# Kernel tuning notes

Hardware: AMD Instinct MI355X
Metric: run time of the kernel (lower is better)

## Reference

```python
import jax, jax.numpy as jnp
import numpy as np

FF = 2          # freqfold
HALF_FF = 1     # ff // 2

def _fold_k(t, G, ff):
    # t: [N, G, D] -> real/imag each [N, nband, G*ff]
    N, _, D = t.shape
    Df = D // 2
    nband = Df // ff
    t = jnp.swapaxes(t, -1, -2)  # [N, D, G]
    def fold(x):  # x: [N, Df, G]
        x = x.reshape(N, nband, ff, G).transpose(0, 2, 1, 3)  # [N, ff, nband, G]
        return x.reshape(N, nband, G * ff)
    return fold(t[:, :Df, :]), fold(t[:, Df:, :])

def _fold_q(t, G, groups, ff):
    # t: [N, H, D] with H = G*groups -> real/imag each [N, groups, nband, G*ff]
    N, H, D = t.shape
    Df = D // 2
    nband = Df // ff
    t = t.reshape(N, G, groups, D).transpose(0, 2, 1, 3)  # [N, groups, G, D]
    t = jnp.swapaxes(t, -1, -2)                            # [N, groups, D, G]
    def fold(x):  # x: [N, groups, Df, G]
        x = x.reshape(N, groups, nband, ff, G).transpose(0, 1, 3, 2, 4)  # [N, groups, ff, nband, G]
        return x.reshape(N, groups, nband, G * ff)
    return fold(t[:, :, :Df, :]), fold(t[:, :, Df:, :])

def setup_inputs() -> dict:
    key = jax.random.key(0)
    ks = jax.random.split(key, 8)
    N, H, G, D, r = 8192, 32, 8, 128, 4
    ff = FF
    nband = D // (2 * ff)
    gff = G * ff
    nope_in = G * D - D // 2
    return {
        "q": jax.random.normal(ks[0], (N, H, D), jnp.float32),
        "k": jax.random.normal(ks[1], (N, G, D), jnp.float32),
        "v": jax.random.normal(ks[2], (N, G, D), jnp.float32),
        "q_orig": jax.random.normal(ks[3], (N, H, D), jnp.float32),
        "k_orig": jax.random.normal(ks[4], (N, G, D), jnp.float32),
        "qk_index_proj": 0.02 * jax.random.normal(ks[5], (nband, gff, gff), jnp.float32),
        "qk_nope_proj_w": 0.02 * jax.random.normal(ks[6], (D // 2, nope_in), jnp.float32),
        "v_transform": 0.02 * jax.random.normal(ks[7], (H, D, r), jnp.float32),
    }

def reference(q, k, v, q_orig, k_orig, qk_index_proj, qk_nope_proj_w, v_transform):
    N, H, D = q.shape
    G = k.shape[1]
    groups = H // G
    ff, half_ff = FF, HALF_FF
    nband = D // (2 * ff)
    nope_cols = G * ff - half_ff
    qk_w = qk_index_proj

    # ---- rope path (post-RoPE q, k) ----
    kr_re, kr_im = _fold_k(k, G, ff)
    kr_re_p = jnp.einsum('bnf,nfr->bnr', kr_re, qk_w)
    kr_im_p = jnp.einsum('bnf,nfr->bnr', kr_im, qk_w)
    index_k_rope = jnp.concatenate([
        kr_re_p[:, :, :half_ff].reshape(N, nband * half_ff),
        kr_im_p[:, :, :half_ff].reshape(N, nband * half_ff)], axis=-1)

    qr_re, qr_im = _fold_q(q, G, groups, ff)
    qr_re_p = jnp.einsum('tgnf,nfr->tgnr', qr_re, qk_w)
    qr_im_p = jnp.einsum('tgnf,nfr->tgnr', qr_im, qk_w)
    index_q_rope = jnp.concatenate([
        qr_re_p[:, :, :, :half_ff].reshape(N, groups, nband * half_ff),
        qr_im_p[:, :, :, :half_ff].reshape(N, groups, nband * half_ff)], axis=-1)

    # ---- nope path (pre-RoPE q_orig, k_orig) ----
    kn_re, kn_im = _fold_k(k_orig, G, ff)
    kn_re_p = jnp.einsum('bnf,nfr->bnr', kn_re, qk_w)
    kn_im_p = jnp.einsum('bnf,nfr->bnr', kn_im, qk_w)
    k_nope_rotary = jnp.concatenate([
        kn_re_p[:, :, half_ff:].reshape(N, nband * nope_cols),
        kn_im_p[:, :, half_ff:].reshape(N, nband * nope_cols)], axis=-1)
    k_nope_lr = k_nope_rotary @ qk_nope_proj_w.T
    index_k = jnp.concatenate([index_k_rope, k_nope_lr], axis=-1)  # [N, D]

    qn_re, qn_im = _fold_q(q_orig, G, groups, ff)
    qn_re_p = jnp.einsum('tgnf,nfr->tgnr', qn_re, qk_w)
    qn_im_p = jnp.einsum('tgnf,nfr->tgnr', qn_im, qk_w)
    q_nope_rotary = jnp.concatenate([
        qn_re_p[:, :, :, half_ff:].reshape(N, groups, nband * nope_cols),
        qn_im_p[:, :, :, half_ff:].reshape(N, groups, nband * nope_cols)], axis=-1)
    q_nope_lr = q_nope_rotary @ qk_nope_proj_w.T
    index_q = jnp.concatenate([index_q_rope, q_nope_lr], axis=-1)  # [N, groups, D]

    # ---- per-head weights from V ----
    r = v_transform.shape[-1]
    v_h = jnp.repeat(v, groups, axis=1)  # [N, H, D]
    w = jnp.einsum('nhd,hdr->nhr', v_h, v_transform)
    w = w.reshape(N, G, groups, r).transpose(0, 2, 1, 3).reshape(N, groups, G * r)
    weights = jnp.linalg.norm(w.astype(jnp.float32), axis=-1)  # [N, groups]

    return index_q, index_k, weights
```

## Files before the change

### kernel.cpp

```cpp
#include <hip/hip_runtime.h>
#include <math.h>

namespace {
constexpr int N_TOK  = 8192;
constexpr int GROUPS = 4;
constexpr int D      = 128;
}

typedef short v8s __attribute__((ext_vector_type(8)));
typedef float v4f __attribute__((ext_vector_type(4)));

__device__ __forceinline__ short f2bf(float f) {
    union { float f; unsigned u; } x; x.f = f;
    unsigned r = x.u + 0x7FFFu + ((x.u >> 16) & 1u);
    return (short)(r >> 16);
}

__global__ __launch_bounds__(256)
void build_MT(const float* __restrict__ widx,
              const float* __restrict__ wn,
              short* __restrict__ MT)
{
    const int idx = blockIdx.x * 256 + threadIdx.x;
    const int col = idx >> 10;
    const int kk  = idx & 1023;
    const int g   = kk >> 7;
    const int dp  = kk & 127;
    const int part = dp >> 6;
    const int dpp  = dp & 63;
    const int B    = (dpp & 1) * 16 + (dpp >> 2);
    const int c    = g + 8 * ((dpp >> 1) & 1);

    float val;
    if (col < 64) {
        val = (col == part * 32 + B) ? widx[B * 256 + c * 16] : 0.f;
    } else {
        const int d2 = col - 64;
        const float* wrow = wn + d2 * 960 + part * 480 + B * 15;
        const float* wi   = widx + B * 256 + c * 16;
        float s = 0.f;
#pragma unroll
        for (int o = 1; o < 16; ++o) s += wi[o] * wrow[o - 1];
        val = s;
    }
    MT[idx] = f2bf(val);
}

__global__ __launch_bounds__(256)
void gemm_kernel(const float* __restrict__ q,
                 const float* __restrict__ k,
                 const float* __restrict__ q_orig,
                 const float* __restrict__ k_orig,
                 const short* __restrict__ MT,
                 float* __restrict__ out_iq,
                 float* __restrict__ out_ik)
{
    const int lane = threadIdx.x & 63;
    const int wave = threadIdx.x >> 6;
    const int m    = lane & 15;
    const int quad = lane >> 4;
    const int base_row = blockIdx.x * 64 + wave * 16;

    const int row = base_row + m;
    const int n   = row / 5;
    const int jj  = row - n * 5;
    const bool isq = (jj < 4);
    const float* ropep = isq ? (q      + n * 4096 + jj * 128) : (k      + n * 1024);
    const float* nopep = isq ? (q_orig + n * 4096 + jj * 128) : (k_orig + n * 1024);

    const short* bbase = MT + m * 1024;

    v4f acc[8];
#pragma unroll
    for (int t = 0; t < 8; ++t) acc[t] = (v4f){0.f, 0.f, 0.f, 0.f};

#pragma unroll 2
    for (int ks = 0; ks < 32; ++ks) {
        const int kk   = ks * 32 + quad * 8;
        const int offA = isq ? ((kk >> 7) * 512 + (kk & 127)) : kk;
        const float4 r0 = *(const float4*)(ropep + offA);
        const float4 r1 = *(const float4*)(ropep + offA + 4);
        const float4 n0 = *(const float4*)(nopep + offA);
        const float4 n1 = *(const float4*)(nopep + offA + 4);
        v8s ar, an;
        ar[0] = f2bf(r0.x); ar[1] = f2bf(r0.y); ar[2] = f2bf(r0.z); ar[3] = f2bf(r0.w);
        ar[4] = f2bf(r1.x); ar[5] = f2bf(r1.y); ar[6] = f2bf(r1.z); ar[7] = f2bf(r1.w);
        an[0] = f2bf(n0.x); an[1] = f2bf(n0.y); an[2] = f2bf(n0.z); an[3] = f2bf(n0.w);
        an[4] = f2bf(n1.x); an[5] = f2bf(n1.y); an[6] = f2bf(n1.z); an[7] = f2bf(n1.w);

        const short* bp = bbase + kk;
#pragma unroll
        for (int t = 0; t < 8; ++t) {
            const v8s b = *(const v8s*)(bp + t * 16384);
            acc[t] = __builtin_amdgcn_mfma_f32_16x16x32_bf16(
                         (t < 4) ? ar : an, b, acc[t], 0, 0, 0);
        }
    }

#pragma unroll
    for (int t = 0; t < 8; ++t) {
        const int col = t * 16 + m;
#pragma unroll
        for (int i = 0; i < 4; ++i) {
            const int r2  = base_row + quad * 4 + i;
            const int n2  = r2 / 5;
            const int jj2 = r2 - n2 * 5;
            float* dst = (jj2 < 4) ? (out_iq + n2 * 512 + jj2 * 128)
                                   : (out_ik + n2 * 128);
            dst[col] = acc[t][i];
        }
    }
}

__global__ __launch_bounds__(256)
void weights_kernel(const float* __restrict__ v,
                    const float* __restrict__ vt,
                    float* __restrict__ out_w)
{
    __shared__ float s_wsq[2][128];
    const int half = threadIdx.x >> 7;
    const int tid  = threadIdx.x & 127;
    const int tok  = blockIdx.x * 2 + half;
    const int h  = tid >> 2;
    const int rr = tid & 3;
    const int g  = h >> 2;
    const float* vrow = v  + tok * 1024 + g * 128;
    const float* vtp  = vt + h * 512 + rr;
    float acc = 0.f;
#pragma unroll 8
    for (int d = 0; d < 128; ++d) acc += vrow[d] * vtp[d * 4];
    s_wsq[half][tid] = acc * acc;
    __syncthreads();
    if (tid < 4) {
        float s = 0.f;
#pragma unroll
        for (int g2 = 0; g2 < 8; ++g2)
#pragma unroll
            for (int r2 = 0; r2 < 4; ++r2)
                s += s_wsq[half][(g2 * 4 + tid) * 4 + r2];
        out_w[tok * 4 + tid] = sqrtf(s);
    }
}

extern "C" void kernel_launch(void* const* d_in, const int* in_sizes, int n_in,
                              void* d_out, int out_size, void* d_ws, size_t ws_size,
                              hipStream_t stream) {
    const float* q      = (const float*)d_in[0];
    const float* k      = (const float*)d_in[1];
    const float* v      = (const float*)d_in[2];
    const float* q_orig = (const float*)d_in[3];
    const float* k_orig = (const float*)d_in[4];
    const float* widx   = (const float*)d_in[5];
    const float* wn     = (const float*)d_in[6];
    const float* vt     = (const float*)d_in[7];

    float* out_iq = (float*)d_out;
    float* out_ik = out_iq + (size_t)N_TOK * GROUPS * D;
    float* out_w  = out_ik + (size_t)N_TOK * D;

    short* MT = (short*)d_ws;

    hipLaunchKernelGGL(build_MT, dim3(512), dim3(256), 0, stream, widx, wn, MT);
    hipLaunchKernelGGL(gemm_kernel, dim3(640), dim3(256), 0, stream,
                       q, k, q_orig, k_orig, MT, out_iq, out_ik);
    hipLaunchKernelGGL(weights_kernel, dim3(4096), dim3(256), 0, stream,
                       v, vt, out_w);
}
```

Before: 471.0 us.

## Split GEMM output columns across blocks and stage v_transform in LDS for weights

The GEMM kernel now launches twice as many blocks, and each block computes only the rope half or only the nope half of the output columns. This halves per-wave accumulators and A loads to raise occupancy and parallelism, at the cost of reading the shared row index math twice. The weights kernel is rewritten to load all of v_transform into shared memory once per block (XOR-swizzled to avoid bank conflicts), compute four rank outputs per thread with float4 loads, and handle 16 tokens per block. This cuts the redundant global reads of v_transform. The 64 KB LDS footprint may limit how many blocks fit on a compute unit.

```diff
diff --git a/kernel.cpp b/kernel.cpp
--- a/kernel.cpp
+++ b/kernel.cpp
@@ -46,7 +46,7 @@
     MT[idx] = f2bf(val);
 }
 
-__global__ __launch_bounds__(256)
+__global__ __launch_bounds__(256, 4)
 void gemm_kernel(const float* __restrict__ q,
                  const float* __restrict__ k,
                  const float* __restrict__ q_orig,
@@ -59,47 +59,44 @@
     const int wave = threadIdx.x >> 6;
     const int m    = lane & 15;
     const int quad = lane >> 4;
-    const int base_row = blockIdx.x * 64 + wave * 16;
+    const int half = blockIdx.x & 1;
+    const int base_row = (blockIdx.x >> 1) * 64 + wave * 16;
 
     const int row = base_row + m;
     const int n   = row / 5;
     const int jj  = row - n * 5;
     const bool isq = (jj < 4);
-    const float* ropep = isq ? (q      + n * 4096 + jj * 128) : (k      + n * 1024);
-    const float* nopep = isq ? (q_orig + n * 4096 + jj * 128) : (k_orig + n * 1024);
-
-    const short* bbase = MT + m * 1024;
-
-    v4f acc[8];
-#pragma unroll
-    for (int t = 0; t < 8; ++t) acc[t] = (v4f){0.f, 0.f, 0.f, 0.f};
-
-#pragma unroll 2
+    const float* ap;
+    if (half == 0) ap = isq ? (q      + n * 4096 + jj * 128) : (k      + n * 1024);
+    else           ap = isq ? (q_orig + n * 4096 + jj * 128) : (k_orig + n * 1024);
+
+    const short* bbase = MT + (half * 64 + m) * 1024;
+
+    v4f acc[4];
+#pragma unroll
+    for (int t = 0; t < 4; ++t) acc[t] = (v4f){0.f, 0.f, 0.f, 0.f};
+
+#pragma unroll 4
     for (int ks = 0; ks < 32; ++ks) {
         const int kk   = ks * 32 + quad * 8;
         const int offA = isq ? ((kk >> 7) * 512 + (kk & 127)) : kk;
-        const float4 r0 = *(const float4*)(ropep + offA);
-        const float4 r1 = *(const float4*)(ropep + offA + 4);
-        const float4 n0 = *(const float4*)(nopep + offA);
-        const float4 n1 = *(const float4*)(nopep + offA + 4);
-        v8s ar, an;
-        ar[0] = f2bf(r0.x); ar[1] = f2bf(r0.y); ar[2] = f2bf(r0.z); ar[3] = f2bf(r0.w);
-        ar[4] = f2bf(r1.x); ar[5] = f2bf(r1.y); ar[6] = f2bf(r1.z); ar[7] = f2bf(r1.w);
-        an[0] = f2bf(n0.x); an[1] = f2bf(n0.y); an[2] = f2bf(n0.z); an[3] = f2bf(n0.w);
-        an[4] = f2bf(n1.x); an[5] = f2bf(n1.y); an[6] = f2bf(n1.z); an[7] = f2bf(n1.w);
+        const float4 r0 = *(const float4*)(ap + offA);
+        const float4 r1 = *(const float4*)(ap + offA + 4);
+        v8s a;
+        a[0] = f2bf(r0.x); a[1] = f2bf(r0.y); a[2] = f2bf(r0.z); a[3] = f2bf(r0.w);
+        a[4] = f2bf(r1.x); a[5] = f2bf(r1.y); a[6] = f2bf(r1.z); a[7] = f2bf(r1.w);
 
         const short* bp = bbase + kk;
 #pragma unroll
-        for (int t = 0; t < 8; ++t) {
+        for (int t = 0; t < 4; ++t) {
             const v8s b = *(const v8s*)(bp + t * 16384);
-            acc[t] = __builtin_amdgcn_mfma_f32_16x16x32_bf16(
-                         (t < 4) ? ar : an, b, acc[t], 0, 0, 0);
-        }
-    }
-
-#pragma unroll
-    for (int t = 0; t < 8; ++t) {
-        const int col = t * 16 + m;
+            acc[t] = __builtin_amdgcn_mfma_f32_16x16x32_bf16(a, b, acc[t], 0, 0, 0);
+        }
+    }
+
+#pragma unroll
+    for (int t = 0; t < 4; ++t) {
+        const int col = half * 64 + t * 16 + m;
 #pragma unroll
         for (int i = 0; i < 4; ++i) {
             const int r2  = base_row + quad * 4 + i;
@@ -112,33 +109,68 @@
     }
 }
 
-__global__ __launch_bounds__(256)
+__global__ __launch_bounds__(512)
 void weights_kernel(const float* __restrict__ v,
                     const float* __restrict__ vt,
                     float* __restrict__ out_w)
 {
-    __shared__ float s_wsq[2][128];
-    const int half = threadIdx.x >> 7;
-    const int tid  = threadIdx.x & 127;
-    const int tok  = blockIdx.x * 2 + half;
-    const int h  = tid >> 2;
-    const int rr = tid & 3;
-    const int g  = h >> 2;
-    const float* vrow = v  + tok * 1024 + g * 128;
-    const float* vtp  = vt + h * 512 + rr;
-    float acc = 0.f;
+    __shared__ float4 s_vt[4096];
+    const int tid = threadIdx.x;
+
+    const float4* vt4 = (const float4*)vt;
+#pragma unroll
+    for (int i0 = 0; i0 < 8; ++i0) {
+        const int i   = i0 * 512 + tid;
+        const int hh  = i >> 7;
+        const int low = i & 127;
+        s_vt[(i & ~127) | (low ^ (hh & 7))] = vt4[i];
+    }
+    __syncthreads();
+
+    const int tok_l = tid & 15;
+    const int h     = tid >> 4;
+    const int g     = h >> 2;
+    const int sw    = h & 7;
+    const int token = blockIdx.x * 16 + tok_l;
+
+    const float4* vrow = (const float4*)(v + token * 1024 + g * 128);
+    const float4* wrow = s_vt + h * 128;
+
+    float ax = 0.f, ay = 0.f, az = 0.f, aw = 0.f;
 #pragma unroll 8
-    for (int d = 0; d < 128; ++d) acc += vrow[d] * vtp[d * 4];
-    s_wsq[half][tid] = acc * acc;
+    for (int d4 = 0; d4 < 32; ++d4) {
+        const float4 vv = vrow[d4];
+        {
+            const float4 w0 = wrow[(d4 * 4 + 0) ^ sw];
+            ax += vv.x * w0.x; ay += vv.x * w0.y; az += vv.x * w0.z; aw += vv.x * w0.w;
+        }
+        {
+            const float4 w1 = wrow[(d4 * 4 + 1) ^ sw];
+            ax += vv.y * w1.x; ay += vv.y * w1.y; az += vv.y * w1.z; aw += vv.y * w1.w;
+        }
+        {
+            const float4 w2 = wrow[(d4 * 4 + 2) ^ sw];
+            ax += vv.z * w2.x; ay += vv.z * w2.y; az += vv.z * w2.z; aw += vv.z * w2.w;
+        }
+        {
+            const float4 w3 = wrow[(d4 * 4 + 3) ^ sw];
+            ax += vv.w * w3.x; ay += vv.w * w3.y; az += vv.w * w3.z; aw += vv.w * w3.w;
+        }
+    }
+    const float s = ax * ax + ay * ay + az * az + aw * aw;
+
     __syncthreads();
-    if (tid < 4) {
-        float s = 0.f;
-#pragma unroll
-        for (int g2 = 0; g2 < 8; ++g2)
-#pragma unroll
-            for (int r2 = 0; r2 < 4; ++r2)
-                s += s_wsq[half][(g2 * 4 + tid) * 4 + r2];
-        out_w[tok * 4 + tid] = sqrtf(s);
+    float* s_red = (float*)s_vt;
+    s_red[tok_l * 32 + h] = s;
+    __syncthreads();
+    if (tid < 64) {
+        const int tok = tid & 15;
+        const int j   = tid >> 4;
+        const float* p = s_red + tok * 32 + j;
+        float t = 0.f;
+#pragma unroll
+        for (int g2 = 0; g2 < 8; ++g2) t += p[g2 * 4];
+        out_w[(blockIdx.x * 16 + tok) * 4 + j] = sqrtf(t);
     }
 }
 
@@ -161,8 +193,8 @@
     short* MT = (short*)d_ws;
 
     hipLaunchKernelGGL(build_MT, dim3(512), dim3(256), 0, stream, widx, wn, MT);
-    hipLaunchKernelGGL(gemm_kernel, dim3(640), dim3(256), 0, stream,
+    hipLaunchKernelGGL(gemm_kernel, dim3(1280), dim3(256), 0, stream,
                        q, k, q_orig, k_orig, MT, out_iq, out_ik);
-    hipLaunchKernelGGL(weights_kernel, dim3(4096), dim3(256), 0, stream,
+    hipLaunchKernelGGL(weights_kernel, dim3(512), dim3(512), 0, stream,
                        v, vt, out_w);
 }
```

After: 390.2 us. 17.2% less time.
